# Kernel tuning notes

Hardware: AMD Instinct MI355X
Metric: run time of the kernel (lower is better)

## Reference

```python
import jax, jax.numpy as jnp
import numpy as np

B, S, H, L = 64, 512, 768, 9


def setup_inputs() -> dict:
    key = jax.random.key(0)
    k0, k1, k2, k3, k4, k5, k6 = jax.random.split(key, 7)
    hidden = jax.random.normal(k0, (B, S, H), dtype=jnp.float32)
    W = jax.random.normal(k1, (L, H), dtype=jnp.float32) * 0.02
    b = jnp.zeros((L,), dtype=jnp.float32)
    start_transitions = jax.random.uniform(k2, (L,), minval=-0.1, maxval=0.1)
    end_transitions = jax.random.uniform(k3, (L,), minval=-0.1, maxval=0.1)
    transitions = jax.random.uniform(k4, (L, L), minval=-0.1, maxval=0.1)
    # variable-length sequences (position 0 always valid), like real padded batches
    lens = jax.random.randint(k5, (B,), S // 2, S + 1)
    attention_mask = jnp.arange(S)[None, :] < lens[:, None]  # (B,S) bool
    labels = jax.random.randint(k6, (B, S), 0, L).astype(jnp.int32)
    return dict(hidden=hidden, W=W, b=b, start_transitions=start_transitions,
                end_transitions=end_transitions, transitions=transitions,
                labels=labels, attention_mask=attention_mask)


def _crf_neg_log_likelihood(feats, labels, mask, start, end, trans):
    """feats (B,S,L) emissions; labels (B,S) int; mask (B,S) bool. Returns scalar mean NLL."""
    fdt = feats.dtype
    # ---- log denominator: forward algorithm as a scan over time ----
    fT = jnp.swapaxes(feats, 0, 1)  # (S,B,L)
    mT = jnp.swapaxes(mask, 0, 1)   # (S,B)
    alpha0 = start + fT[0]          # (B,L)

    def step(alpha, xs):
        f_t, m_t = xs
        # (B,L_prev,1) + (L_prev,L_next) + (B,1,L_next) -> logsumexp over prev
        new = jax.nn.logsumexp(alpha[:, :, None] + trans[None, :, :] + f_t[:, None, :], axis=1)
        return jnp.where(m_t[:, None], new, alpha), None

    alpha, _ = jax.lax.scan(step, alpha0, (fT[1:], mT[1:]))
    log_den = jax.nn.logsumexp(alpha + end, axis=1)  # (B,)

    # ---- log numerator: score of the gold path, fully vectorized ----
    emit = jnp.take_along_axis(feats, labels[..., None].astype(jnp.int32), axis=2)[..., 0]  # (B,S)
    tr = trans[labels[:, :-1], labels[:, 1:]]  # (B,S-1)
    score = start[labels[:, 0]] + emit[:, 0]
    score = score + jnp.sum((tr + emit[:, 1:]) * mask[:, 1:].astype(fdt), axis=1)
    lens = jnp.sum(mask.astype(jnp.int32), axis=1) - 1  # index of last valid token
    last_tags = jnp.take_along_axis(labels, lens[:, None], axis=1)[:, 0]
    score = score + end[last_tags]

    return jnp.mean(log_den - score)


def reference(hidden, W, b, start_transitions, end_transitions, transitions, labels, attention_mask):
    # hidden2label linear (dropout is identity in eval mode)
    feats = jnp.einsum('bsh,lh->bsl', hidden, W) + b  # (B,S,L)
    return _crf_neg_log_likelihood(feats, labels, attention_mask,
                                   start_transitions, end_transitions, transitions)
```

## Files before the change

kernel.cpp:

```cpp
#include <hip/hip_runtime.h>
#include <hip/hip_bf16.h>

#define BB 64
#define SS 512
#define HH 768
#define LL 9
#define CL 16
#define NC (SS / CL)
#define NEG (-1e30f)

#define EXP2F(x) exp2f(x)
#define LOG2F(x) __log2f(x)

static __device__ __forceinline__ float dot4(float4 a, float4 b) {
    return a.x * b.x + a.y * b.y + a.z * b.z + a.w * b.w;
}

static __device__ __forceinline__ float max9(const float* v) {
    float m1 = fmaxf(fmaxf(v[0], v[1]), v[2]);
    float m2 = fmaxf(fmaxf(v[3], v[4]), v[5]);
    float m3 = fmaxf(fmaxf(v[6], v[7]), v[8]);
    return fmaxf(fmaxf(m1, m2), m3);
}

static __device__ __forceinline__ float sum9exp(const float* v, float mx) {
    float e0 = EXP2F(v[0] - mx), e1 = EXP2F(v[1] - mx), e2 = EXP2F(v[2] - mx);
    float e3 = EXP2F(v[3] - mx), e4 = EXP2F(v[4] - mx), e5 = EXP2F(v[5] - mx);
    float e6 = EXP2F(v[6] - mx), e7 = EXP2F(v[7] - mx), e8 = EXP2F(v[8] - mx);
    return ((e0 + e1) + (e2 + e3)) + (((e4 + e5) + (e6 + e7)) + e8);
}

template <int CTRL>
static __device__ __forceinline__ float dpp_add(float v) {
    return v + __int_as_float(
        __builtin_amdgcn_update_dpp(0, __float_as_int(v), CTRL, 0xF, 0xF, true));
}

static __device__ __forceinline__ float wave_sum64(float v) {
    v = dpp_add<0xB1>(v);
    v = dpp_add<0x4E>(v);
    v = dpp_add<0x124>(v);
    v = dpp_add<0x128>(v);
    v += __shfl_xor(v, 16);
    v += __shfl_xor(v, 32);
    return v;
}

__global__ __launch_bounds__(256, 2)
void fused_kernel(const float* __restrict__ hidden,
                  const float* __restrict__ W,
                  const float* __restrict__ bias,
                  const float* __restrict__ start_t,
                  const float* __restrict__ end_t,
                  const float* __restrict__ trans,
                  const int* __restrict__ labels,
                  const int* __restrict__ mask,
                  float* __restrict__ Q,
                  float* __restrict__ A0,
                  float* __restrict__ Sc,
                  float* __restrict__ out0) {
    const int bid  = blockIdx.x;
    const int b    = bid >> 5;
    const int c    = bid & (NC - 1);
    const int tid  = threadIdx.x;
    const int lane = tid & 63;
    const int wv   = tid >> 6;

    if (bid == 0 && tid == 0) out0[0] = 0.f;

    __shared__ float fsl[CL][12];
    __shared__ float Pb[2][LL][16];

    const int bS     = b * SS;
    const int t_base = c * CL;

    const int i  = tid >> 4;
    const int j  = tid & 15;
    const int jc = j < LL ? j : LL - 1;
    const float INV_LN2 = 1.4426950408889634f;

    float trC[LL];
#pragma unroll
    for (int k = 0; k < LL; ++k) trC[k] = trans[k * LL + jc] * INV_LN2;

    const int off   = (c == 0) ? 1 : 0;
    const int steps = CL - off;
    const int t0    = t_base + off;

    int na = 0;
#pragma unroll
    for (int u = 0; u < CL; ++u)
        na += (u < steps && mask[bS + t0 + u] != 0) ? 1 : 0;

    int mt = 0, lc = 0, lp = 0, mnext = 0;
    const int t_sc = t_base + lane;
    if (wv == 3 && lane < CL) {
        mt    = mask[bS + t_sc];
        lc    = labels[bS + t_sc];
        lp    = (t_sc >= 1) ? labels[bS + t_sc - 1] : 0;
        mnext = (t_sc == SS - 1) ? 0 : mask[bS + t_sc + 1];
    }

    float4 wreg[3][LL];
#pragma unroll
    for (int c3 = 0; c3 < 3; ++c3)
#pragma unroll
        for (int l = 0; l < LL; ++l)
            wreg[c3][l] = *(const float4*)(W + l * HH + c3 * 256 + (lane << 2));
    const float bv = bias[lane < LL ? lane : 0];

    const float* hbase = hidden + ((size_t)bS + t_base) * HH;
#pragma unroll
    for (int pair = 0; pair < 2; ++pair) {
        const int r0 = wv * 4 + pair * 2;
        const int r1 = r0 + 1;
        const float4* h0p = (const float4*)(hbase + (size_t)r0 * HH);
        const float4* h1p = (const float4*)(hbase + (size_t)r1 * HH);
        float4 a0 = h0p[lane], a1 = h0p[64 + lane], a2 = h0p[128 + lane];
        float4 b0 = h1p[lane], b1 = h1p[64 + lane], b2 = h1p[128 + lane];
        float accA[LL], accB[LL];
#pragma unroll
        for (int l = 0; l < LL; ++l) {
            accA[l] = dot4(a0, wreg[0][l]) + dot4(a1, wreg[1][l]) + dot4(a2, wreg[2][l]);
            accB[l] = dot4(b0, wreg[0][l]) + dot4(b1, wreg[1][l]) + dot4(b2, wreg[2][l]);
        }
        float outA = 0.f, outB = 0.f;
#pragma unroll
        for (int l = 0; l < LL; ++l) {
            float sA = wave_sum64(accA[l]);
            float sB = wave_sum64(accB[l]);
            if (lane == l) { outA = sA; outB = sB; }
        }
        if (lane < LL) {
            fsl[r0][lane] = outA + bv;
            fsl[r1][lane] = outB + bv;
        }
    }

    float P = (i == j) ? 0.f : NEG;
    if (tid < 144) Pb[0][i][j] = P;
    __syncthreads();

    if (wv == 3 && lane < CL) {
        float sc = 0.f;
        if (t_sc >= 1 && mt) sc += trans[lp * LL + lc] + fsl[lane][lc];
        if (t_sc == 0)       sc += start_t[lc] + fsl[0][lc];
        if (mt && !mnext)    sc += end_t[lc];
#pragma unroll
        for (int o = 1; o < CL; o <<= 1) sc += __shfl_xor(sc, o);
        if (lane == 0) Sc[bid] = sc;
        if (c == 0 && lane < LL)
            A0[b * 16 + lane] = (start_t[lane] + fsl[0][lane]) * INV_LN2;
    }

    float fsr[CL];
#pragma unroll
    for (int u = 0; u < CL; ++u)
        fsr[u] = (u < steps) ? fsl[u + off][jc] * INV_LN2 : 0.f;

#pragma unroll
    for (int s = 0; s < CL; ++s) {
        if (s < na) {
            if (tid < 144) {
                const float* row = &Pb[s & 1][i][0];
                float v[LL];
#pragma unroll
                for (int k = 0; k < LL; ++k) v[k] = row[k] + trC[k];
                const float mx  = max9(v);
                const float sum = sum9exp(v, mx);
                P = mx + LOG2F(sum) + fsr[s];
                Pb[(s + 1) & 1][i][j] = P;
            }
        }
        __syncthreads();
    }

    if (tid < 144 && j < LL)
        Q[(size_t)bid * (LL * LL) + i * LL + j] = P;
}

__global__ __launch_bounds__(64, 1)
void combine_kernel(const float* __restrict__ Q,
                    const float* __restrict__ A0,
                    const float* __restrict__ Sc,
                    const float* __restrict__ end_t,
                    float* __restrict__ out) {
    const int b    = blockIdx.x;
    const int lane = threadIdx.x;
    const int j    = lane < LL ? lane : LL - 1;
    const float INV_LN2 = 1.4426950408889634f;
    const float LN2     = 0.6931471805599453f;

    float score = (lane < NC) ? Sc[b * NC + lane] : 0.f;
#pragma unroll
    for (int o = 1; o < 64; o <<= 1) score += __shfl_xor(score, o);

    float alpha[LL];
#pragma unroll
    for (int k = 0; k < LL; ++k) alpha[k] = A0[b * 16 + k];

    const float* Qb = Q + (size_t)b * NC * (LL * LL);
    float qcol[LL], qnext[LL];
#pragma unroll
    for (int k = 0; k < LL; ++k) qnext[k] = Qb[k * LL + j];
    for (int cc = 0; cc < NC; ++cc) {
#pragma unroll
        for (int k = 0; k < LL; ++k) qcol[k] = qnext[k];
        if (cc + 1 < NC) {
            const float* Qn = Qb + (size_t)(cc + 1) * (LL * LL);
#pragma unroll
            for (int k = 0; k < LL; ++k) qnext[k] = Qn[k * LL + j];
        }
        float v[LL];
#pragma unroll
        for (int k = 0; k < LL; ++k) v[k] = alpha[k] + qcol[k];
        const float mx  = max9(v);
        const float sum = sum9exp(v, mx);
        const float anew = mx + LOG2F(sum);
#pragma unroll
        for (int k = 0; k < LL; ++k)
            alpha[k] = __uint_as_float(__builtin_amdgcn_readlane(__float_as_uint(anew), k));
    }

    float v[LL];
#pragma unroll
    for (int k = 0; k < LL; ++k) v[k] = alpha[k] + end_t[k] * INV_LN2;
    const float mx  = max9(v);
    const float sum = sum9exp(v, mx);
    const float log_den = (mx + LOG2F(sum)) * LN2;

    if (lane == 0)
        atomicAdd(out, (log_den - score) * (1.0f / BB));
}

extern "C" void kernel_launch(void* const* d_in, const int* in_sizes, int n_in,
                              void* d_out, int out_size, void* d_ws, size_t ws_size,
                              hipStream_t stream) {
    const float* hidden = (const float*)d_in[0];
    const float* W      = (const float*)d_in[1];
    const float* bias   = (const float*)d_in[2];
    const float* startT = (const float*)d_in[3];
    const float* endT   = (const float*)d_in[4];
    const float* trans  = (const float*)d_in[5];
    const int*   labels = (const int*)d_in[6];
    const int*   mask   = (const int*)d_in[7];

    float* Q  = (float*)d_ws;
    float* A0 = Q + (size_t)BB * NC * LL * LL;
    float* Sc = A0 + BB * 16;

    fused_kernel<<<dim3(BB * NC), dim3(256), 0, stream>>>(
        hidden, W, bias, startT, endT, trans, labels, mask, Q, A0, Sc, (float*)d_out);
    combine_kernel<<<dim3(BB), dim3(64), 0, stream>>>(Q, A0, Sc, endT, (float*)d_out);
}
```

Before: 192.3 us.

## Halve chunk length, drop cross-group shuffles via LDS partial sums, raise occupancy

Chunk length goes from 16 to 8 timesteps, so twice as many blocks (4096) each run a shorter serial logsumexp chain, and the combine kernel walks 64 chunks per batch instead of 32. The emission projection now handles one row pair per wave and reduces only within 16-lane groups using DPP. The four group partials go to LDS and are summed when read, which removes the cross-row shuffles. Launch bounds ask for 3 blocks per CU. The cost is a longer sequential combine chain, more 9x9 chunk matrices written to and read from global memory, and W being reloaded by twice as many blocks.

Result: no change. 191.7 us (-0.3%).

```diff
diff --git a/kernel.cpp b/kernel.cpp
--- a/kernel.cpp
+++ b/kernel.cpp
@@ -5,7 +5,7 @@
 #define SS 512
 #define HH 768
 #define LL 9
-#define CL 16
+#define CL 8
 #define NC (SS / CL)
 #define NEG (-1e30f)
 
@@ -36,17 +36,20 @@
         __builtin_amdgcn_update_dpp(0, __float_as_int(v), CTRL, 0xF, 0xF, true));
 }
 
-static __device__ __forceinline__ float wave_sum64(float v) {
+static __device__ __forceinline__ float group_sum16(float v) {
     v = dpp_add<0xB1>(v);
     v = dpp_add<0x4E>(v);
     v = dpp_add<0x124>(v);
     v = dpp_add<0x128>(v);
-    v += __shfl_xor(v, 16);
-    v += __shfl_xor(v, 32);
     return v;
 }
 
-__global__ __launch_bounds__(256, 2)
+static __device__ __forceinline__ float lds_sum4(const float* p) {
+    float4 q = *(const float4*)p;
+    return (q.x + q.y) + (q.z + q.w);
+}
+
+__global__ __launch_bounds__(256, 3)
 void fused_kernel(const float* __restrict__ hidden,
                   const float* __restrict__ W,
                   const float* __restrict__ bias,
@@ -60,7 +63,7 @@
                   float* __restrict__ Sc,
                   float* __restrict__ out0) {
     const int bid  = blockIdx.x;
-    const int b    = bid >> 5;
+    const int b    = bid >> 6;
     const int c    = bid & (NC - 1);
     const int tid  = threadIdx.x;
     const int lane = tid & 63;
@@ -68,20 +71,21 @@
 
     if (bid == 0 && tid == 0) out0[0] = 0.f;
 
-    __shared__ float fsl[CL][12];
+    __shared__ float fsl4[CL][LL][4];
     __shared__ float Pb[2][LL][16];
 
     const int bS     = b * SS;
     const int t_base = c * CL;
+    const float INV_LN2 = 1.4426950408889634f;
 
     const int i  = tid >> 4;
     const int j  = tid & 15;
     const int jc = j < LL ? j : LL - 1;
-    const float INV_LN2 = 1.4426950408889634f;
 
     float trC[LL];
 #pragma unroll
     for (int k = 0; k < LL; ++k) trC[k] = trans[k * LL + jc] * INV_LN2;
+    const float bjc = bias[jc];
 
     const int off   = (c == 0) ? 1 : 0;
     const int steps = CL - off;
@@ -107,34 +111,33 @@
 #pragma unroll
         for (int l = 0; l < LL; ++l)
             wreg[c3][l] = *(const float4*)(W + l * HH + c3 * 256 + (lane << 2));
-    const float bv = bias[lane < LL ? lane : 0];
 
     const float* hbase = hidden + ((size_t)bS + t_base) * HH;
-#pragma unroll
-    for (int pair = 0; pair < 2; ++pair) {
-        const int r0 = wv * 4 + pair * 2;
-        const int r1 = r0 + 1;
-        const float4* h0p = (const float4*)(hbase + (size_t)r0 * HH);
-        const float4* h1p = (const float4*)(hbase + (size_t)r1 * HH);
-        float4 a0 = h0p[lane], a1 = h0p[64 + lane], a2 = h0p[128 + lane];
-        float4 b0 = h1p[lane], b1 = h1p[64 + lane], b2 = h1p[128 + lane];
-        float accA[LL], accB[LL];
-#pragma unroll
-        for (int l = 0; l < LL; ++l) {
-            accA[l] = dot4(a0, wreg[0][l]) + dot4(a1, wreg[1][l]) + dot4(a2, wreg[2][l]);
-            accB[l] = dot4(b0, wreg[0][l]) + dot4(b1, wreg[1][l]) + dot4(b2, wreg[2][l]);
-        }
-        float outA = 0.f, outB = 0.f;
-#pragma unroll
-        for (int l = 0; l < LL; ++l) {
-            float sA = wave_sum64(accA[l]);
-            float sB = wave_sum64(accB[l]);
-            if (lane == l) { outA = sA; outB = sB; }
-        }
-        if (lane < LL) {
-            fsl[r0][lane] = outA + bv;
-            fsl[r1][lane] = outB + bv;
-        }
+    const int r0 = wv * 2, r1 = r0 + 1;
+    const float4* h0p = (const float4*)(hbase + (size_t)r0 * HH);
+    const float4* h1p = (const float4*)(hbase + (size_t)r1 * HH);
+    float4 a0 = h0p[lane], a1 = h0p[64 + lane], a2 = h0p[128 + lane];
+    float4 b0 = h1p[lane], b1 = h1p[64 + lane], b2 = h1p[128 + lane];
+
+    float accA[LL], accB[LL];
+#pragma unroll
+    for (int l = 0; l < LL; ++l) {
+        accA[l] = dot4(a0, wreg[0][l]) + dot4(a1, wreg[1][l]) + dot4(a2, wreg[2][l]);
+        accB[l] = dot4(b0, wreg[0][l]) + dot4(b1, wreg[1][l]) + dot4(b2, wreg[2][l]);
+    }
+
+    const int g  = lane >> 4;
+    const int sl = lane & 15;
+    float selA = 0.f, selB = 0.f;
+#pragma unroll
+    for (int l = 0; l < LL; ++l) {
+        float rA = group_sum16(accA[l]);
+        float rB = group_sum16(accB[l]);
+        if (sl == l) { selA = rA; selB = rB; }
+    }
+    if (sl < LL) {
+        fsl4[r0][sl][g] = selA;
+        fsl4[r1][sl][g] = selB;
     }
 
     float P = (i == j) ? 0.f : NEG;
@@ -143,20 +146,23 @@
 
     if (wv == 3 && lane < CL) {
         float sc = 0.f;
-        if (t_sc >= 1 && mt) sc += trans[lp * LL + lc] + fsl[lane][lc];
-        if (t_sc == 0)       sc += start_t[lc] + fsl[0][lc];
-        if (mt && !mnext)    sc += end_t[lc];
+        if (t_sc >= 1 && mt)
+            sc += trans[lp * LL + lc] + lds_sum4(&fsl4[lane][lc][0]) + bias[lc];
+        if (t_sc == 0)
+            sc += start_t[lc] + lds_sum4(&fsl4[0][lc][0]) + bias[lc];
+        if (mt && !mnext) sc += end_t[lc];
 #pragma unroll
         for (int o = 1; o < CL; o <<= 1) sc += __shfl_xor(sc, o);
         if (lane == 0) Sc[bid] = sc;
-        if (c == 0 && lane < LL)
-            A0[b * 16 + lane] = (start_t[lane] + fsl[0][lane]) * INV_LN2;
-    }
+    }
+    if (c == 0 && wv == 2 && lane < LL)
+        A0[b * 16 + lane] =
+            (start_t[lane] + lds_sum4(&fsl4[0][lane][0]) + bias[lane]) * INV_LN2;
 
     float fsr[CL];
 #pragma unroll
     for (int u = 0; u < CL; ++u)
-        fsr[u] = (u < steps) ? fsl[u + off][jc] * INV_LN2 : 0.f;
+        fsr[u] = (u < steps) ? (lds_sum4(&fsl4[u + off][jc][0]) + bjc) * INV_LN2 : 0.f;
 
 #pragma unroll
     for (int s = 0; s < CL; ++s) {
@@ -191,7 +197,7 @@
     const float INV_LN2 = 1.4426950408889634f;
     const float LN2     = 0.6931471805599453f;
 
-    float score = (lane < NC) ? Sc[b * NC + lane] : 0.f;
+    float score = Sc[b * NC + lane];
 #pragma unroll
     for (int o = 1; o < 64; o <<= 1) score += __shfl_xor(score, o);
 
```
